# Kernel tuning notes

Measured on AMD Instinct MI355X. Metric: run time of the kernel, lower is better.

## Reference

```python
import jax, jax.numpy as jnp
import numpy as np

D, E, FF = 512, 8, 4 * 512
BS, H, W = 2, 32, 32
T = BS * H * W


def setup_inputs() -> dict:
    key = jax.random.key(0)
    ks = jax.random.split(key, 12)
    s = lambda fan_in: 1.0 / np.sqrt(fan_in)
    return {
        "x": jax.random.normal(ks[0], (BS, D, H, W), dtype=jnp.float32),
        "Wg": jax.random.normal(ks[1], (D, E), dtype=jnp.float32) * s(D),
        "bg": jnp.zeros((E,), dtype=jnp.float32),
        "Wn": jax.random.normal(ks[2], (D, E), dtype=jnp.float32) * s(D),
        "bn": jnp.zeros((E,), dtype=jnp.float32),
        "W1": jax.random.normal(ks[3], (E, D, FF), dtype=jnp.float32) * s(D),
        "b1": jnp.zeros((E, FF), dtype=jnp.float32),
        "W2": jax.random.normal(ks[4], (E, FF, D), dtype=jnp.float32) * s(FF),
        "b2": jnp.zeros((E, D), dtype=jnp.float32),
        "noise_eps": jax.random.normal(ks[5], (T, E), dtype=jnp.float32),
        "top_k": 2,
    }


def reference(x, Wg, bg, Wn, bn, W1, b1, W2, b2, noise_eps, top_k):
    bs, d, h, w = x.shape
    tokens = x.transpose(0, 2, 3, 1).reshape(-1, d)  # [T, d]
    t = tokens.shape[0]
    # Noisy top-k router
    logits = tokens @ Wg + bg                                  # [T, E]
    noise = noise_eps * jax.nn.softplus(tokens @ Wn + bn)      # [T, E]
    noisy = logits + noise
    top_v, top_i = jax.lax.top_k(noisy, top_k)                 # [T, k]
    sparse = jnp.full_like(noisy, -jnp.inf)
    sparse = sparse.at[jnp.arange(t)[:, None], top_i].set(top_v)
    gates = jax.nn.softmax(sparse, axis=-1)                    # [T, E], zero off top-k
    # Expert MLPs (dense over experts; gates zero-out non-selected)
    hdn = jax.nn.relu(jnp.einsum("td,edf->tef", tokens, W1) + b1)  # [T, E, 4d]
    out_e = jnp.einsum("tef,efd->ted", hdn, W2) + b2               # [T, E, d]
    out = jnp.einsum("te,ted->td", gates, out_e)                   # combine
    return out.reshape(bs, h, w, d).transpose(0, 3, 1, 2)
```

## Files before the change

kernel.cpp:

```cpp
#include <hip/hip_runtime.h>
#include <hip/hip_bf16.h>
#include <math.h>

#define DD  512
#define EE  8
#define FFD 2048
#define TT  2048
#define HWH 1024

typedef __bf16 b16x8 __attribute__((ext_vector_type(8)));
typedef float  f32x4 __attribute__((ext_vector_type(4)));

__device__ __forceinline__ unsigned short f2bf(float f) {
    unsigned u = __builtin_bit_cast(unsigned, f);
    u = (u + 0x7FFFu + ((u >> 16) & 1u)) >> 16;
    return (unsigned short)u;
}

__device__ __forceinline__ void gload16(const void* g, void* l) {
    __builtin_amdgcn_global_load_lds(
        (const __attribute__((address_space(1))) void*)g,
        (__attribute__((address_space(3))) void*)l, 16, 0, 0);
}

__global__ __launch_bounds__(256) void moe_transpose(
    const float* __restrict__ W1, const float* __restrict__ W2,
    const float* __restrict__ x,
    unsigned short* __restrict__ W1t, unsigned short* __restrict__ W2t,
    unsigned short* __restrict__ xb)
{
    int which = blockIdx.z, e = blockIdx.y;
    const float* in; unsigned short* out; int R, C;
    if (which == 0)      { R = DD;  C = FFD; in = W1 + (size_t)e*DD*FFD; out = W1t + (size_t)e*FFD*DD; }
    else if (which == 1) { R = FFD; C = DD;  in = W2 + (size_t)e*FFD*DD; out = W2t + (size_t)e*DD*FFD; }
    else { if (e >= 2) return; R = DD; C = HWH; in = x + (size_t)e*DD*HWH; out = xb + (size_t)e*HWH*DD; }
    int tilesC = C >> 6;
    if ((int)blockIdx.x >= (R >> 6) * tilesC) return;
    int tr = (blockIdx.x / tilesC) << 6, tc = (blockIdx.x % tilesC) << 6;
    __shared__ float ld[64][65];
    int ty = threadIdx.x >> 4, tx = threadIdx.x & 15;
    #pragma unroll
    for (int i = 0; i < 4; ++i) {
        const float4 v = *(const float4*)&in[(size_t)(tr + ty + i*16)*C + tc + tx*4];
        ld[ty + i*16][tx*4+0] = v.x; ld[ty + i*16][tx*4+1] = v.y;
        ld[ty + i*16][tx*4+2] = v.z; ld[ty + i*16][tx*4+3] = v.w;
    }
    __syncthreads();
    #pragma unroll
    for (int i = 0; i < 4; ++i) {
        int c = ty + i*16;
        unsigned o0 = f2bf(ld[tx*4+0][c]) | ((unsigned)f2bf(ld[tx*4+1][c]) << 16);
        unsigned o1 = f2bf(ld[tx*4+2][c]) | ((unsigned)f2bf(ld[tx*4+3][c]) << 16);
        *(uint2*)&out[(size_t)(tc + c)*R + tr + tx*4] = make_uint2(o0, o1);
    }
}

__global__ __launch_bounds__(256) void moe_router_part(
    const float* __restrict__ x, const float* __restrict__ Wg,
    const float* __restrict__ Wn, float* __restrict__ part)
{
    int u = threadIdx.x & 63;
    int q = threadIdx.x >> 6;
    int tt = blockIdx.x, dc = blockIdx.y;
    int t = tt * 64 + u;
    int b = t >> 10, hw = t & 1023;
    const float* xp = x + (size_t)b * DD * HWH + hw;
    int d0 = dc * 64 + q * 16;
    float accL[EE], accN[EE];
    #pragma unroll
    for (int e = 0; e < EE; ++e) { accL[e] = 0.f; accN[e] = 0.f; }
    #pragma unroll
    for (int i = 0; i < 16; ++i) {
        int d = d0 + i;
        float tv = xp[(size_t)d * HWH];
        #pragma unroll
        for (int e = 0; e < EE; ++e) {
            accL[e] = fmaf(tv, Wg[d * EE + e], accL[e]);
            accN[e] = fmaf(tv, Wn[d * EE + e], accN[e]);
        }
    }
    __shared__ float s[4][64][16];
    #pragma unroll
    for (int e = 0; e < EE; ++e) { s[q][u][e] = accL[e]; s[q][u][e + 8] = accN[e]; }
    __syncthreads();
    int idx = threadIdx.x * 4;
    int ot = idx >> 4, oc = idx & 15;
    float4 v;
    v.x = s[0][ot][oc+0] + s[1][ot][oc+0] + s[2][ot][oc+0] + s[3][ot][oc+0];
    v.y = s[0][ot][oc+1] + s[1][ot][oc+1] + s[2][ot][oc+1] + s[3][ot][oc+1];
    v.z = s[0][ot][oc+2] + s[1][ot][oc+2] + s[2][ot][oc+2] + s[3][ot][oc+2];
    v.w = s[0][ot][oc+3] + s[1][ot][oc+3] + s[2][ot][oc+3] + s[3][ot][oc+3];
    *(float4*)&part[((size_t)dc * TT + tt * 64 + ot) * 16 + oc] = v;
}

__global__ __launch_bounds__(256) void moe_router_topk(
    const float* __restrict__ part,
    const float* __restrict__ bg, const float* __restrict__ bn,
    const float* __restrict__ neps,
    int* __restrict__ cnt, int* __restrict__ pair0, int* __restrict__ pair1,
    int* __restrict__ ltok, float* __restrict__ lgate)
{
    int t = blockIdx.x * 256 + threadIdx.x;
    float L[EE], N[EE];
    #pragma unroll
    for (int e = 0; e < EE; ++e) { L[e] = bg[e]; N[e] = bn[e]; }
    #pragma unroll
    for (int dc = 0; dc < 8; ++dc) {
        const float* p = &part[((size_t)dc * TT + t) * 16];
        float4 a0 = *(const float4*)&p[0];
        float4 a1 = *(const float4*)&p[4];
        float4 a2 = *(const float4*)&p[8];
        float4 a3 = *(const float4*)&p[12];
        L[0] += a0.x; L[1] += a0.y; L[2] += a0.z; L[3] += a0.w;
        L[4] += a1.x; L[5] += a1.y; L[6] += a1.z; L[7] += a1.w;
        N[0] += a2.x; N[1] += a2.y; N[2] += a2.z; N[3] += a2.w;
        N[4] += a3.x; N[5] += a3.y; N[6] += a3.z; N[7] += a3.w;
    }
    float noisy[EE];
    #pragma unroll
    for (int e = 0; e < EE; ++e) {
        float sp = fmaxf(N[e], 0.f) + log1pf(expf(-fabsf(N[e])));
        noisy[e] = L[e] + neps[t * EE + e] * sp;
    }
    int e0 = 0; float v0 = noisy[0];
    #pragma unroll
    for (int e = 1; e < EE; ++e) if (noisy[e] > v0) { v0 = noisy[e]; e0 = e; }
    int e1 = (e0 == 0) ? 1 : 0; float v1 = noisy[e1];
    #pragma unroll
    for (int e = 0; e < EE; ++e)
        if (e != e0 && e != e1 && noisy[e] > v1) { v1 = noisy[e]; e1 = e; }
    float ex  = expf(v1 - v0);
    float inv = 1.f / (1.f + ex);
    float g0 = inv, g1 = ex * inv;
    int p0 = atomicAdd(&cnt[e0], 1);
    int p1 = atomicAdd(&cnt[e1], 1);
    ltok[e0 * TT + p0] = t; lgate[e0 * TT + p0] = g0;
    ltok[e1 * TT + p1] = t; lgate[e1 * TT + p1] = g1;
    pair0[t] = (e0 << 16) | p0;
    pair1[t] = (e1 << 16) | p1;
}

__global__ void moe_prefix(const int* __restrict__ cnt, int* __restrict__ seg)
{
    if (threadIdx.x == 0) {
        int s = 0;
        for (int e = 0; e < EE; ++e) { seg[e] = s; s += cnt[e]; }
        seg[EE] = s;
    }
}

__global__ __launch_bounds__(256, 3) void moe_gemm1(
    const unsigned short* __restrict__ xb, const unsigned short* __restrict__ W1t,
    const float* __restrict__ b1, const int* __restrict__ cnt,
    const int* __restrict__ seg, const int* __restrict__ ltok,
    unsigned short* __restrict__ Hbuf)
{
    int e = blockIdx.x, mt = blockIdx.y, nt = blockIdx.z;
    int ce = cnt[e];
    if (mt * 64 >= ce) return;
    int s0 = seg[e];
    const unsigned short* Be = W1t + (size_t)e * FFD * DD;
    __shared__ unsigned short As[2][64 * 64];
    __shared__ unsigned short Bs[2][128 * 64];
    int tid = threadIdx.x, lane = tid & 63, wv = tid >> 6;

    int srow = lane >> 3, schunk = lane & 7;
    int srcoff = ((schunk ^ srow) << 3);

    size_t aoff[2]; int ards[2];
    #pragma unroll
    for (int c = 0; c < 2; ++c) {
        int r0 = (c*4 + wv)*8;
        int ri = mt*64 + r0 + srow;
        int tok = ltok[e * TT + (ri < ce ? ri : 0)];
        aoff[c] = (size_t)tok * DD + srcoff;
        ards[c] = r0 * 64;
    }
    size_t boff[4]; int brds[4];
    #pragma unroll
    for (int c = 0; c < 4; ++c) {
        int r0 = (c*4 + wv)*8;
        boff[c] = (size_t)(nt*128 + r0 + srow) * DD + srcoff;
        brds[c] = r0 * 64;
    }

    int frow = lane & 15, fk = (lane >> 4) * 8;
    int am = (wv >> 1) * 32, bnn = (wv & 1) * 64;
    int rx = (frow & 7) << 3;

    f32x4 acc[2][4];
    f32x4 zero = {0.f, 0.f, 0.f, 0.f};
    #pragma unroll
    for (int m = 0; m < 2; ++m)
        #pragma unroll
        for (int n = 0; n < 4; ++n) acc[m][n] = zero;

    #pragma unroll
    for (int c = 0; c < 2; ++c) gload16(&xb[aoff[c]], &As[0][ards[c]]);
    #pragma unroll
    for (int c = 0; c < 4; ++c) gload16(&Be[boff[c]], &Bs[0][brds[c]]);
    __syncthreads();

    int cur = 0;
    for (int t = 0; t < 8; ++t) {
        if (t < 7) {
            int kk = (t + 1) * 64;
            #pragma unroll
            for (int c = 0; c < 2; ++c) gload16(&xb[aoff[c] + kk], &As[cur^1][ards[c]]);
            #pragma unroll
            for (int c = 0; c < 4; ++c) gload16(&Be[boff[c] + kk], &Bs[cur^1][brds[c]]);
        }
        #pragma unroll
        for (int k2 = 0; k2 < 64; k2 += 32) {
            b16x8 af[2], bf[4];
            #pragma unroll
            for (int m = 0; m < 2; ++m)
                af[m] = *(const b16x8*)&As[cur][(am + m*16 + frow)*64 + ((k2 + fk) ^ rx)];
            #pragma unroll
            for (int n = 0; n < 4; ++n)
                bf[n] = *(const b16x8*)&Bs[cur][(bnn + n*16 + frow)*64 + ((k2 + fk) ^ rx)];
            #pragma unroll
            for (int m = 0; m < 2; ++m)
                #pragma unroll
                for (int n = 0; n < 4; ++n)
                    acc[m][n] = __builtin_amdgcn_mfma_f32_16x16x32_bf16(af[m], bf[n], acc[m][n], 0, 0, 0);
        }
        __syncthreads();
        cur ^= 1;
    }

    int crow = (lane >> 4) * 4;
    #pragma unroll
    for (int m = 0; m < 2; ++m) {
        #pragma unroll
        for (int i = 0; i < 4; ++i) {
            int r = mt*64 + am + m*16 + crow + i;
            if (r < ce) {
                size_t hrow = (size_t)(s0 + r) * FFD;
                #pragma unroll
                for (int n = 0; n < 4; ++n) {
                    int col = nt*128 + bnn + n*16 + frow;
                    float v = acc[m][n][i] + b1[e * FFD + col];
                    Hbuf[hrow + col] = f2bf(fmaxf(v, 0.f));
                }
            }
        }
    }
}

__global__ __launch_bounds__(256, 3) void moe_gemm2(
    const unsigned short* __restrict__ Hbuf, const unsigned short* __restrict__ W2t,
    const int* __restrict__ cnt, const int* __restrict__ seg,
    float* __restrict__ P4)
{
    int e = blockIdx.x, mt = blockIdx.y;
    int split = blockIdx.z >> 2, nt = blockIdx.z & 3;
    int ce = cnt[e];
    if (mt * 64 >= ce) return;
    int s0 = seg[e];
    int kbase = split * 512;
    const unsigned short* Be = W2t + (size_t)e * DD * FFD;
    __shared__ unsigned short As[2][64 * 64];
    __shared__ unsigned short Bs[2][128 * 64];
    int tid = threadIdx.x, lane = tid & 63, wv = tid >> 6;

    int srow = lane >> 3, schunk = lane & 7;
    int srcoff = ((schunk ^ srow) << 3);

    size_t aoff[2]; int ards[2];
    #pragma unroll
    for (int c = 0; c < 2; ++c) {
        int r0 = (c*4 + wv)*8;
        int g = s0 + mt*64 + r0 + srow; if (g > 4095) g = 4095;
        aoff[c] = (size_t)g * FFD + kbase + srcoff;
        ards[c] = r0 * 64;
    }
    size_t boff[4]; int brds[4];
    #pragma unroll
    for (int c = 0; c < 4; ++c) {
        int r0 = (c*4 + wv)*8;
        boff[c] = (size_t)(nt*128 + r0 + srow) * FFD + kbase + srcoff;
        brds[c] = r0 * 64;
    }

    int frow = lane & 15, fk = (lane >> 4) * 8;
    int am = (wv >> 1) * 32, bnn = (wv & 1) * 64;
    int rx = (frow & 7) << 3;

    f32x4 acc[2][4];
    f32x4 zero = {0.f, 0.f, 0.f, 0.f};
    #pragma unroll
    for (int m = 0; m < 2; ++m)
        #pragma unroll
        for (int n = 0; n < 4; ++n) acc[m][n] = zero;

    #pragma unroll
    for (int c = 0; c < 2; ++c) gload16(&Hbuf[aoff[c]], &As[0][ards[c]]);
    #pragma unroll
    for (int c = 0; c < 4; ++c) gload16(&Be[boff[c]], &Bs[0][brds[c]]);
    __syncthreads();

    int cur = 0;
    for (int t = 0; t < 8; ++t) {
        if (t < 7) {
            int kk = (t + 1) * 64;
            #pragma unroll
            for (int c = 0; c < 2; ++c) gload16(&Hbuf[aoff[c] + kk], &As[cur^1][ards[c]]);
            #pragma unroll
            for (int c = 0; c < 4; ++c) gload16(&Be[boff[c] + kk], &Bs[cur^1][brds[c]]);
        }
        #pragma unroll
        for (int k2 = 0; k2 < 64; k2 += 32) {
            b16x8 af[2], bf[4];
            #pragma unroll
            for (int m = 0; m < 2; ++m)
                af[m] = *(const b16x8*)&As[cur][(am + m*16 + frow)*64 + ((k2 + fk) ^ rx)];
            #pragma unroll
            for (int n = 0; n < 4; ++n)
                bf[n] = *(const b16x8*)&Bs[cur][(bnn + n*16 + frow)*64 + ((k2 + fk) ^ rx)];
            #pragma unroll
            for (int m = 0; m < 2; ++m)
                #pragma unroll
                for (int n = 0; n < 4; ++n)
                    acc[m][n] = __builtin_amdgcn_mfma_f32_16x16x32_bf16(af[m], bf[n], acc[m][n], 0, 0, 0);
        }
        __syncthreads();
        cur ^= 1;
    }

    int crow = (lane >> 4) * 4;
    float* Pw = P4 + (size_t)split * 4096 * DD;
    #pragma unroll
    for (int m = 0; m < 2; ++m) {
        #pragma unroll
        for (int i = 0; i < 4; ++i) {
            int r = mt*64 + am + m*16 + crow + i;
            if (r < ce) {
                size_t prow = (size_t)(s0 + r) * DD;
                #pragma unroll
                for (int n = 0; n < 4; ++n) {
                    int col = nt*128 + bnn + n*16 + frow;
                    Pw[prow + col] = acc[m][n][i];
                }
            }
        }
    }
}

__global__ __launch_bounds__(256) void moe_combine(
    const int* __restrict__ pair0, const int* __restrict__ pair1,
    const int* __restrict__ seg, const float* __restrict__ lgate,
    const float* __restrict__ b2, const float* __restrict__ P4,
    float* __restrict__ out)
{
    __shared__ float tile[32][68];
    int tid = threadIdx.x;
    int ti = blockIdx.x, dc = blockIdx.y;
    int ty = tid >> 3, tx = tid & 7;
    int t = ti * 32 + ty;
    int a0 = pair0[t], a1 = pair1[t];
    int e0 = a0 >> 16, sl0 = a0 & 0xFFFF;
    int e1 = a1 >> 16, sl1 = a1 & 0xFFFF;
    int p0 = seg[e0] + sl0, p1 = seg[e1] + sl1;
    float g0 = lgate[e0 * TT + sl0], g1 = lgate[e1 * TT + sl1];
    int d0 = dc * 64 + tx * 8;
    f32x4 s0v[2] = {{0,0,0,0},{0,0,0,0}}, s1v[2] = {{0,0,0,0},{0,0,0,0}};
    #pragma unroll
    for (int s = 0; s < 4; ++s) {
        const f32x4* r0p = (const f32x4*)(P4 + ((size_t)s * 4096 + p0) * DD + d0);
        const f32x4* r1p = (const f32x4*)(P4 + ((size_t)s * 4096 + p1) * DD + d0);
        s0v[0] += r0p[0]; s0v[1] += r0p[1];
        s1v[0] += r1p[0]; s1v[1] += r1p[1];
    }
    const f32x4* b0p = (const f32x4*)(b2 + e0 * DD + d0);
    const f32x4* b1p = (const f32x4*)(b2 + e1 * DD + d0);
    #pragma unroll
    for (int q = 0; q < 2; ++q) {
        f32x4 v = g0 * (s0v[q] + b0p[q]) + g1 * (s1v[q] + b1p[q]);
        *(f32x4*)&tile[ty][tx*8 + q*4] = v;
    }
    __syncthreads();
    int dy = tid >> 2, hx = tid & 3;
    int b = (ti * 32) >> 10, hw0 = (ti * 32) & 1023;
    size_t obase = ((size_t)(b * DD + dc * 64 + dy)) * HWH + hw0;
    #pragma unroll
    for (int q = 0; q < 2; ++q) {
        int j = hx * 8 + q * 4;
        float4 w;
        w.x = tile[j + 0][dy];
        w.y = tile[j + 1][dy];
        w.z = tile[j + 2][dy];
        w.w = tile[j + 3][dy];
        *(float4*)&out[obase + j] = w;
    }
}

extern "C" void kernel_launch(void* const* d_in, const int* in_sizes, int n_in,
                              void* d_out, int out_size, void* d_ws, size_t ws_size,
                              hipStream_t stream)
{
    const float* x    = (const float*)d_in[0];
    const float* Wg   = (const float*)d_in[1];
    const float* bg   = (const float*)d_in[2];
    const float* Wn   = (const float*)d_in[3];
    const float* bn   = (const float*)d_in[4];
    const float* W1   = (const float*)d_in[5];
    const float* b1   = (const float*)d_in[6];
    const float* W2   = (const float*)d_in[7];
    const float* b2   = (const float*)d_in[8];
    const float* neps = (const float*)d_in[9];

    char* ws = (char*)d_ws;
    int*   cnt   = (int*)(ws + 0);
    int*   seg   = (int*)(ws + 256);
    int*   pair0 = (int*)(ws + 512);
    int*   pair1 = (int*)(ws + 8704);
    int*   ltok  = (int*)(ws + 32768);
    float* lgate = (float*)(ws + 98304);
    float* part  = (float*)(ws + 163840);
    unsigned short* xb   = (unsigned short*)(ws + 1212416);
    unsigned short* Hbuf = (unsigned short*)(ws + 3309568);
    unsigned short* W1t  = (unsigned short*)(ws + 20086784);
    unsigned short* W2t  = (unsigned short*)(ws + 36864000);
    float*          P4   = (float*)(ws + 53641216);

    hipMemsetAsync(cnt, 0, 32, stream);
    moe_transpose<<<dim3(256, 8, 3), 256, 0, stream>>>(W1, W2, x, W1t, W2t, xb);
    moe_router_part<<<dim3(TT / 64, 8), 256, 0, stream>>>(x, Wg, Wn, part);
    moe_router_topk<<<TT / 256, 256, 0, stream>>>(part, bg, bn, neps,
                                                  cnt, pair0, pair1, ltok, lgate);
    moe_prefix<<<1, 64, 0, stream>>>(cnt, seg);
    moe_gemm1<<<dim3(EE, 32, 16), 256, 0, stream>>>(xb, W1t, b1, cnt, seg, ltok, Hbuf);
    moe_gemm2<<<dim3(EE, 32, 16), 256, 0, stream>>>(Hbuf, W2t, cnt, seg, P4);
    moe_combine<<<dim3(TT / 32, 8), 256, 0, stream>>>(pair0, pair1, seg, lgate, b2, P4, (float*)d_out);
}
```

Before: 106.3 us.

## Merge router into prep kernel, shrink GEMM K-tile, remap block order

Folds the router partial-sum kernel into the transpose kernel as an extra z-slice, which removes one launch. Both expert GEMMs move from a 64-wide K tile to a 32-wide one with a new XOR swizzle. That halves LDS use and lets launch bounds ask for 4 blocks per CU instead of 3. The grid becomes 1D with a remapped block index so consecutive blocks share an M tile across experts and N tiles, aiming at better L2 reuse and load balance. The cost is twice as many barrier-separated K iterations and a shallower prefetch per stage.

```diff
diff --git a/kernel.cpp b/kernel.cpp
--- a/kernel.cpp
+++ b/kernel.cpp
@@ -23,13 +23,54 @@
         (__attribute__((address_space(3))) void*)l, 16, 0, 0);
 }
 
-__global__ __launch_bounds__(256) void moe_transpose(
+__global__ __launch_bounds__(256) void moe_prep(
     const float* __restrict__ W1, const float* __restrict__ W2,
     const float* __restrict__ x,
     unsigned short* __restrict__ W1t, unsigned short* __restrict__ W2t,
-    unsigned short* __restrict__ xb)
-{
+    unsigned short* __restrict__ xb,
+    const float* __restrict__ Wg, const float* __restrict__ Wn,
+    float* __restrict__ part)
+{
+    __shared__ float ld[64][65];
     int which = blockIdx.z, e = blockIdx.y;
+
+    if (which == 3) {
+        if (blockIdx.x >= 32) return;
+        int u = threadIdx.x & 63;
+        int q = threadIdx.x >> 6;
+        int tt = blockIdx.x, dc = e;
+        int t = tt * 64 + u;
+        int b = t >> 10, hw = t & 1023;
+        const float* xp = x + (size_t)b * DD * HWH + hw;
+        int d0 = dc * 64 + q * 16;
+        float accL[EE], accN[EE];
+        #pragma unroll
+        for (int k = 0; k < EE; ++k) { accL[k] = 0.f; accN[k] = 0.f; }
+        #pragma unroll
+        for (int i = 0; i < 16; ++i) {
+            int d = d0 + i;
+            float tv = xp[(size_t)d * HWH];
+            #pragma unroll
+            for (int k = 0; k < EE; ++k) {
+                accL[k] = fmaf(tv, Wg[d * EE + k], accL[k]);
+                accN[k] = fmaf(tv, Wn[d * EE + k], accN[k]);
+            }
+        }
+        float (*s)[64][16] = (float (*)[64][16])&ld[0][0];
+        #pragma unroll
+        for (int k = 0; k < EE; ++k) { s[q][u][k] = accL[k]; s[q][u][k + 8] = accN[k]; }
+        __syncthreads();
+        int idx = threadIdx.x * 4;
+        int ot = idx >> 4, oc = idx & 15;
+        float4 v;
+        v.x = s[0][ot][oc+0] + s[1][ot][oc+0] + s[2][ot][oc+0] + s[3][ot][oc+0];
+        v.y = s[0][ot][oc+1] + s[1][ot][oc+1] + s[2][ot][oc+1] + s[3][ot][oc+1];
+        v.z = s[0][ot][oc+2] + s[1][ot][oc+2] + s[2][ot][oc+2] + s[3][ot][oc+2];
+        v.w = s[0][ot][oc+3] + s[1][ot][oc+3] + s[2][ot][oc+3] + s[3][ot][oc+3];
+        *(float4*)&part[((size_t)dc * TT + tt * 64 + ot) * 16 + oc] = v;
+        return;
+    }
+
     const float* in; unsigned short* out; int R, C;
     if (which == 0)      { R = DD;  C = FFD; in = W1 + (size_t)e*DD*FFD; out = W1t + (size_t)e*FFD*DD; }
     else if (which == 1) { R = FFD; C = DD;  in = W2 + (size_t)e*FFD*DD; out = W2t + (size_t)e*DD*FFD; }
@@ -37,7 +78,6 @@
     int tilesC = C >> 6;
     if ((int)blockIdx.x >= (R >> 6) * tilesC) return;
     int tr = (blockIdx.x / tilesC) << 6, tc = (blockIdx.x % tilesC) << 6;
-    __shared__ float ld[64][65];
     int ty = threadIdx.x >> 4, tx = threadIdx.x & 15;
     #pragma unroll
     for (int i = 0; i < 4; ++i) {
@@ -53,44 +93,6 @@
         unsigned o1 = f2bf(ld[tx*4+2][c]) | ((unsigned)f2bf(ld[tx*4+3][c]) << 16);
         *(uint2*)&out[(size_t)(tc + c)*R + tr + tx*4] = make_uint2(o0, o1);
     }
-}
-
-__global__ __launch_bounds__(256) void moe_router_part(
-    const float* __restrict__ x, const float* __restrict__ Wg,
-    const float* __restrict__ Wn, float* __restrict__ part)
-{
-    int u = threadIdx.x & 63;
-    int q = threadIdx.x >> 6;
-    int tt = blockIdx.x, dc = blockIdx.y;
-    int t = tt * 64 + u;
-    int b = t >> 10, hw = t & 1023;
-    const float* xp = x + (size_t)b * DD * HWH + hw;
-    int d0 = dc * 64 + q * 16;
-    float accL[EE], accN[EE];
-    #pragma unroll
-    for (int e = 0; e < EE; ++e) { accL[e] = 0.f; accN[e] = 0.f; }
-    #pragma unroll
-    for (int i = 0; i < 16; ++i) {
-        int d = d0 + i;
-        float tv = xp[(size_t)d * HWH];
-        #pragma unroll
-        for (int e = 0; e < EE; ++e) {
-            accL[e] = fmaf(tv, Wg[d * EE + e], accL[e]);
-            accN[e] = fmaf(tv, Wn[d * EE + e], accN[e]);
-        }
-    }
-    __shared__ float s[4][64][16];
-    #pragma unroll
-    for (int e = 0; e < EE; ++e) { s[q][u][e] = accL[e]; s[q][u][e + 8] = accN[e]; }
-    __syncthreads();
-    int idx = threadIdx.x * 4;
-    int ot = idx >> 4, oc = idx & 15;
-    float4 v;
-    v.x = s[0][ot][oc+0] + s[1][ot][oc+0] + s[2][ot][oc+0] + s[3][ot][oc+0];
-    v.y = s[0][ot][oc+1] + s[1][ot][oc+1] + s[2][ot][oc+1] + s[3][ot][oc+1];
-    v.z = s[0][ot][oc+2] + s[1][ot][oc+2] + s[2][ot][oc+2] + s[3][ot][oc+2];
-    v.w = s[0][ot][oc+3] + s[1][ot][oc+3] + s[2][ot][oc+3] + s[3][ot][oc+3];
-    *(float4*)&part[((size_t)dc * TT + tt * 64 + ot) * 16 + oc] = v;
 }
 
 __global__ __launch_bounds__(256) void moe_router_topk(
@@ -149,44 +151,38 @@
     }
 }
 
-__global__ __launch_bounds__(256, 3) void moe_gemm1(
+__global__ __launch_bounds__(256, 4) void moe_gemm1(
     const unsigned short* __restrict__ xb, const unsigned short* __restrict__ W1t,
     const float* __restrict__ b1, const int* __restrict__ cnt,
     const int* __restrict__ seg, const int* __restrict__ ltok,
     unsigned short* __restrict__ Hbuf)
 {
-    int e = blockIdx.x, mt = blockIdx.y, nt = blockIdx.z;
+    int id = blockIdx.x;
+    int c8 = id & 7;
+    int mt = (id >> 3) & 31;
+    int p  = id >> 8;
+    int combo = p * 8 + c8;
+    int e  = combo >> 4;
+    int nt = combo & 15;
     int ce = cnt[e];
     if (mt * 64 >= ce) return;
     int s0 = seg[e];
     const unsigned short* Be = W1t + (size_t)e * FFD * DD;
-    __shared__ unsigned short As[2][64 * 64];
-    __shared__ unsigned short Bs[2][128 * 64];
+    __shared__ unsigned short As[2][64 * 32];
+    __shared__ unsigned short Bs[2][128 * 32];
     int tid = threadIdx.x, lane = tid & 63, wv = tid >> 6;
 
-    int srow = lane >> 3, schunk = lane & 7;
-    int srcoff = ((schunk ^ srow) << 3);
-
-    size_t aoff[2]; int ards[2];
-    #pragma unroll
-    for (int c = 0; c < 2; ++c) {
-        int r0 = (c*4 + wv)*8;
-        int ri = mt*64 + r0 + srow;
-        int tok = ltok[e * TT + (ri < ce ? ri : 0)];
-        aoff[c] = (size_t)tok * DD + srcoff;
-        ards[c] = r0 * 64;
-    }
-    size_t boff[4]; int brds[4];
-    #pragma unroll
-    for (int c = 0; c < 4; ++c) {
-        int r0 = (c*4 + wv)*8;
-        boff[c] = (size_t)(nt*128 + r0 + srow) * DD + srcoff;
-        brds[c] = r0 * 64;
-    }
-
-    int frow = lane & 15, fk = (lane >> 4) * 8;
+    int rA = tid >> 2, cc = tid & 3;
+    int ri = mt * 64 + rA;
+    int tokA = ltok[e * TT + (ri < ce ? ri : 0)];
+    size_t aoff = (size_t)tokA * DD + ((cc ^ ((rA >> 1) & 3)) << 3);
+    int rB0 = rA, rB1 = rA + 64;
+    size_t boff0 = (size_t)(nt*128 + rB0) * DD + ((cc ^ ((rB0 >> 1) & 3)) << 3);
+    size_t boff1 = (size_t)(nt*128 + rB1) * DD + ((cc ^ ((rB1 >> 1) & 3)) << 3);
+    int wb = wv * 512;
+
+    int frow = lane & 15, chR = lane >> 4;
     int am = (wv >> 1) * 32, bnn = (wv & 1) * 64;
-    int rx = (frow & 7) << 3;
 
     f32x4 acc[2][4];
     f32x4 zero = {0.f, 0.f, 0.f, 0.f};
@@ -195,36 +191,35 @@
         #pragma unroll
         for (int n = 0; n < 4; ++n) acc[m][n] = zero;
 
-    #pragma unroll
-    for (int c = 0; c < 2; ++c) gload16(&xb[aoff[c]], &As[0][ards[c]]);
-    #pragma unroll
-    for (int c = 0; c < 4; ++c) gload16(&Be[boff[c]], &Bs[0][brds[c]]);
+    gload16(&xb[aoff], &As[0][wb]);
+    gload16(&Be[boff0], &Bs[0][wb]);
+    gload16(&Be[boff1], &Bs[0][2048 + wb]);
     __syncthreads();
 
     int cur = 0;
-    for (int t = 0; t < 8; ++t) {
-        if (t < 7) {
-            int kk = (t + 1) * 64;
-            #pragma unroll
-            for (int c = 0; c < 2; ++c) gload16(&xb[aoff[c] + kk], &As[cur^1][ards[c]]);
-            #pragma unroll
-            for (int c = 0; c < 4; ++c) gload16(&Be[boff[c] + kk], &Bs[cur^1][brds[c]]);
-        }
-        #pragma unroll
-        for (int k2 = 0; k2 < 64; k2 += 32) {
-            b16x8 af[2], bf[4];
-            #pragma unroll
-            for (int m = 0; m < 2; ++m)
-                af[m] = *(const b16x8*)&As[cur][(am + m*16 + frow)*64 + ((k2 + fk) ^ rx)];
+    for (int t = 0; t < 16; ++t) {
+        if (t < 15) {
+            int kk = (t + 1) * 32;
+            gload16(&xb[aoff + kk], &As[cur^1][wb]);
+            gload16(&Be[boff0 + kk], &Bs[cur^1][wb]);
+            gload16(&Be[boff1 + kk], &Bs[cur^1][2048 + wb]);
+        }
+        b16x8 af[2], bf[4];
+        #pragma unroll
+        for (int m = 0; m < 2; ++m) {
+            int ra = am + m*16 + frow;
+            af[m] = *(const b16x8*)&As[cur][ra*32 + ((chR ^ ((ra>>1)&3)) << 3)];
+        }
+        #pragma unroll
+        for (int n = 0; n < 4; ++n) {
+            int rb = bnn + n*16 + frow;
+            bf[n] = *(const b16x8*)&Bs[cur][rb*32 + ((chR ^ ((rb>>1)&3)) << 3)];
+        }
+        #pragma unroll
+        for (int m = 0; m < 2; ++m)
             #pragma unroll
             for (int n = 0; n < 4; ++n)
-                bf[n] = *(const b16x8*)&Bs[cur][(bnn + n*16 + frow)*64 + ((k2 + fk) ^ rx)];
-            #pragma unroll
-            for (int m = 0; m < 2; ++m)
-                #pragma unroll
-                for (int n = 0; n < 4; ++n)
-                    acc[m][n] = __builtin_amdgcn_mfma_f32_16x16x32_bf16(af[m], bf[n], acc[m][n], 0, 0, 0);
-        }
+                acc[m][n] = __builtin_amdgcn_mfma_f32_16x16x32_bf16(af[m], bf[n], acc[m][n], 0, 0, 0);
         __syncthreads();
         cur ^= 1;
     }
@@ -248,44 +243,38 @@
     }
 }
 
-__global__ __launch_bounds__(256, 3) void moe_gemm2(
+__global__ __launch_bounds__(256, 4) void moe_gemm2(
     const unsigned short* __restrict__ Hbuf, const unsigned short* __restrict__ W2t,
     const int* __restrict__ cnt, const int* __restrict__ seg,
     float* __restrict__ P4)
 {
-    int e = blockIdx.x, mt = blockIdx.y;
-    int split = blockIdx.z >> 2, nt = blockIdx.z & 3;
+    int id = blockIdx.x;
+    int c8 = id & 7;
+    int mt = (id >> 3) & 31;
+    int p  = id >> 8;
+    int combo = p * 8 + c8;
+    int e  = combo >> 4;
+    int z  = combo & 15;
+    int split = z >> 2, nt = z & 3;
     int ce = cnt[e];
     if (mt * 64 >= ce) return;
     int s0 = seg[e];
     int kbase = split * 512;
     const unsigned short* Be = W2t + (size_t)e * DD * FFD;
-    __shared__ unsigned short As[2][64 * 64];
-    __shared__ unsigned short Bs[2][128 * 64];
+    __shared__ unsigned short As[2][64 * 32];
+    __shared__ unsigned short Bs[2][128 * 32];
     int tid = threadIdx.x, lane = tid & 63, wv = tid >> 6;
 
-    int srow = lane >> 3, schunk = lane & 7;
-    int srcoff = ((schunk ^ srow) << 3);
-
-    size_t aoff[2]; int ards[2];
-    #pragma unroll
-    for (int c = 0; c < 2; ++c) {
-        int r0 = (c*4 + wv)*8;
-        int g = s0 + mt*64 + r0 + srow; if (g > 4095) g = 4095;
-        aoff[c] = (size_t)g * FFD + kbase + srcoff;
-        ards[c] = r0 * 64;
-    }
-    size_t boff[4]; int brds[4];
-    #pragma unroll
-    for (int c = 0; c < 4; ++c) {
-        int r0 = (c*4 + wv)*8;
-        boff[c] = (size_t)(nt*128 + r0 + srow) * FFD + kbase + srcoff;
-        brds[c] = r0 * 64;
-    }
-
-    int frow = lane & 15, fk = (lane >> 4) * 8;
+    int rA = tid >> 2, cc = tid & 3;
+    int g = s0 + mt*64 + rA; if (g > 4095) g = 4095;
+    size_t aoff = (size_t)g * FFD + kbase + ((cc ^ ((rA >> 1) & 3)) << 3);
+    int rB0 = rA, rB1 = rA + 64;
+    size_t boff0 = (size_t)(nt*128 + rB0) * FFD + kbase + ((cc ^ ((rB0 >> 1) & 3)) << 3);
+    size_t boff1 = (size_t)(nt*128 + rB1) * FFD + kbase + ((cc ^ ((rB1 >> 1) & 3)) << 3);
+    int wb = wv * 512;
+
+    int frow = lane & 15, chR = lane >> 4;
     int am = (wv >> 1) * 32, bnn = (wv & 1) * 64;
-    int rx = (frow & 7) << 3;
 
     f32x4 acc[2][4];
     f32x4 zero = {0.f, 0.f, 0.f, 0.f};
@@ -294,36 +283,35 @@
         #pragma unroll
         for (int n = 0; n < 4; ++n) acc[m][n] = zero;
 
-    #pragma unroll
-    for (int c = 0; c < 2; ++c) gload16(&Hbuf[aoff[c]], &As[0][ards[c]]);
-    #pragma unroll
-    for (int c = 0; c < 4; ++c) gload16(&Be[boff[c]], &Bs[0][brds[c]]);
+    gload16(&Hbuf[aoff], &As[0][wb]);
+    gload16(&Be[boff0], &Bs[0][wb]);
+    gload16(&Be[boff1], &Bs[0][2048 + wb]);
     __syncthreads();
 
     int cur = 0;
-    for (int t = 0; t < 8; ++t) {
-        if (t < 7) {
-            int kk = (t + 1) * 64;
-            #pragma unroll
-            for (int c = 0; c < 2; ++c) gload16(&Hbuf[aoff[c] + kk], &As[cur^1][ards[c]]);
-            #pragma unroll
-            for (int c = 0; c < 4; ++c) gload16(&Be[boff[c] + kk], &Bs[cur^1][brds[c]]);
-        }
-        #pragma unroll
-        for (int k2 = 0; k2 < 64; k2 += 32) {
-            b16x8 af[2], bf[4];
-            #pragma unroll
-            for (int m = 0; m < 2; ++m)
-                af[m] = *(const b16x8*)&As[cur][(am + m*16 + frow)*64 + ((k2 + fk) ^ rx)];
+    for (int t = 0; t < 16; ++t) {
+        if (t < 15) {
+            int kk = (t + 1) * 32;
+            gload16(&Hbuf[aoff + kk], &As[cur^1][wb]);
+            gload16(&Be[boff0 + kk], &Bs[cur^1][wb]);
+            gload16(&Be[boff1 + kk], &Bs[cur^1][2048 + wb]);
+        }
+        b16x8 af[2], bf[4];
+        #pragma unroll
+        for (int m = 0; m < 2; ++m) {
+            int ra = am + m*16 + frow;
+            af[m] = *(const b16x8*)&As[cur][ra*32 + ((chR ^ ((ra>>1)&3)) << 3)];
+        }
+        #pragma unroll
+        for (int n = 0; n < 4; ++n) {
+            int rb = bnn + n*16 + frow;
+            bf[n] = *(const b16x8*)&Bs[cur][rb*32 + ((chR ^ ((rb>>1)&3)) << 3)];
+        }
+        #pragma unroll
+        for (int m = 0; m < 2; ++m)
             #pragma unroll
             for (int n = 0; n < 4; ++n)
-                bf[n] = *(const b16x8*)&Bs[cur][(bnn + n*16 + frow)*64 + ((k2 + fk) ^ rx)];
-            #pragma unroll
-            for (int m = 0; m < 2; ++m)
-                #pragma unroll
-                for (int n = 0; n < 4; ++n)
-                    acc[m][n] = __builtin_amdgcn_mfma_f32_16x16x32_bf16(af[m], bf[n], acc[m][n], 0, 0, 0);
-        }
+                acc[m][n] = __builtin_amdgcn_mfma_f32_16x16x32_bf16(af[m], bf[n], acc[m][n], 0, 0, 0);
         __syncthreads();
         cur ^= 1;
     }
@@ -425,12 +413,11 @@
     float*          P4   = (float*)(ws + 53641216);
 
     hipMemsetAsync(cnt, 0, 32, stream);
-    moe_transpose<<<dim3(256, 8, 3), 256, 0, stream>>>(W1, W2, x, W1t, W2t, xb);
-    moe_router_part<<<dim3(TT / 64, 8), 256, 0, stream>>>(x, Wg, Wn, part);
+    moe_prep<<<dim3(256, 8, 4), 256, 0, stream>>>(W1, W2, x, W1t, W2t, xb, Wg, Wn, part);
     moe_router_topk<<<TT / 256, 256, 0, stream>>>(part, bg, bn, neps,
                                                   cnt, pair0, pair1, ltok, lgate);
     moe_prefix<<<1, 64, 0, stream>>>(cnt, seg);
-    moe_gemm1<<<dim3(EE, 32, 16), 256, 0, stream>>>(xb, W1t, b1, cnt, seg, ltok, Hbuf);
-    moe_gemm2<<<dim3(EE, 32, 16), 256, 0, stream>>>(Hbuf, W2t, cnt, seg, P4);
+    moe_gemm1<<<4096, 256, 0, stream>>>(xb, W1t, b1, cnt, seg, ltok, Hbuf);
+    moe_gemm2<<<4096, 256, 0, stream>>>(Hbuf, W2t, cnt, seg, P4);
     moe_combine<<<dim3(TT / 32, 8), 256, 0, stream>>>(pair0, pair1, seg, lgate, b2, P4, (float*)d_out);
 }
```

Result: slower. 113.3 us (+6.6%).
